# Kernel tuning notes

Measured on AMD Instinct MI355X. Metric: run time of the kernel, lower is better.

Reference implementation:

```python
import jax, jax.numpy as jnp
import numpy as np

DIM = 16  # scale_size[0] * scale_size[1]
SCALE = DIM ** -0.5


def setup_inputs() -> dict:
    key = jax.random.key(0)
    k1, k2 = jax.random.split(key)
    x = jax.random.normal(k1, (16, 256, 256, 64), dtype=jnp.float32)
    # torch Linear(dim, 2*dim, bias=False): weight shape [32, 16]
    w_qkv = jax.random.normal(k2, (32, 16), dtype=jnp.float32) * (DIM ** -0.5)
    return {"x": x, "w_qkv": w_qkv}


def reference(x, w_qkv):
    B, H, W, C = x.shape
    sh, sw = 4, 4  # scale_size
    # permute to (b, c, h, w) then adaptive avg pool to (4, 4)
    xp = jnp.transpose(x, (0, 3, 1, 2))  # [B, C, H, W]
    pooled = xp.reshape(B, C, sh, H // sh, sw, W // sw).mean(axis=(3, 5))  # [B, C, 4, 4]
    tokens = pooled.reshape(B, C, DIM)  # [B, C, 16]
    # to_qkv: Linear with weight [2*dim, dim] -> x @ W^T, then chunk
    qk = jnp.einsum('bcn,dn->bcd', tokens, w_qkv)  # [B, C, 32]
    q, k = qk[..., :DIM], qk[..., DIM:]  # each [B, C, 16]
    dots = jnp.einsum('bin,bjn->bij', q, k) * SCALE  # [B, C, C]
    attn = jax.nn.softmax(dots, axis=-1)  # [B, C, C]
    out = jnp.einsum('bhwc,btc->bhwt', x, attn)  # [B, H, W, C]
    return jax.nn.gelu(out, approximate=False)
```

## Files before the change

### kernel.cpp

```cpp
#include <hip/hip_runtime.h>
#include <math.h>
#include <cstddef>

#define BB   16
#define HH   256
#define WW   256
#define CC   64
#define NTOK 16
#define NDIM 16

#define PART_FLOATS (BB * NTOK * 16 * CC)
#define FRAG_USHORT_PER_B (8 * 64 * 8)

typedef short s16x8 __attribute__((ext_vector_type(8)));
typedef float f32x4 __attribute__((ext_vector_type(4)));

__device__ __forceinline__ unsigned short f2bf_rne(float f) {
    unsigned int u = __float_as_uint(f);
    return (unsigned short)((u + 0x7fffu + ((u >> 16) & 1u)) >> 16);
}

__global__ __launch_bounds__(256) void pool_partial(const float* __restrict__ x,
                                                    float* __restrict__ part) {
    const int blk = blockIdx.x;
    const int rc  = blk & 15;
    const int n   = (blk >> 4) & 15;
    const int b   = blk >> 8;
    const int ph  = n >> 2, pw = n & 3;
    const int t   = threadIdx.x;
    const int c4  = (t & 15) << 2;
    const int sub = t >> 4;

    const int h0 = ph * 64 + rc * 4;
    const int w0 = pw * 64;
    const float* xb = x + (((size_t)b * HH + h0) * WW + w0) * CC;

    float4 s = make_float4(0.f, 0.f, 0.f, 0.f);
#pragma unroll
    for (int k = 0; k < 16; ++k) {
        const int pos = sub + (k << 4);
        const int row = pos >> 6;
        const int col = pos & 63;
        const float4 v = *(const float4*)(xb + ((size_t)row * WW + col) * CC + c4);
        s.x += v.x; s.y += v.y; s.z += v.z; s.w += v.w;
    }

    __shared__ float lds[16 * 64];
    lds[sub * 64 + c4 + 0] = s.x;
    lds[sub * 64 + c4 + 1] = s.y;
    lds[sub * 64 + c4 + 2] = s.z;
    lds[sub * 64 + c4 + 3] = s.w;
    __syncthreads();

    if (t < 64) {
        float acc = 0.f;
#pragma unroll
        for (int ss = 0; ss < 16; ++ss) acc += lds[ss * 64 + t];
        part[(((size_t)b * NTOK + n) * 16 + rc) * CC + t] = acc;
    }
}

__global__ __launch_bounds__(256) void attn_kernel(const float* __restrict__ part,
                                                   const float* __restrict__ w_qkv,
                                                   unsigned short* __restrict__ fragw) {
    const int b = blockIdx.x;
    const int t = threadIdx.x;

    __shared__ float tok[CC * NDIM];
    __shared__ float ql [CC * NDIM];
    __shared__ float kl [CC * NDIM];
    __shared__ float dl [CC * CC];
    __shared__ float rs [CC];

    const float* pb = part + (size_t)b * NTOK * 16 * CC;

    {
        const int n  = t >> 4;
        const int cq = t & 15;
        float4 a = make_float4(0.f, 0.f, 0.f, 0.f);
#pragma unroll
        for (int rc = 0; rc < 16; ++rc) {
            const float4 v = *(const float4*)(pb + ((size_t)n * 16 + rc) * CC + cq * 4);
            a.x += v.x; a.y += v.y; a.z += v.z; a.w += v.w;
        }
        tok[(cq * 4 + 0) * NDIM + n] = a.x * (1.0f / 4096.0f);
        tok[(cq * 4 + 1) * NDIM + n] = a.y * (1.0f / 4096.0f);
        tok[(cq * 4 + 2) * NDIM + n] = a.z * (1.0f / 4096.0f);
        tok[(cq * 4 + 3) * NDIM + n] = a.w * (1.0f / 4096.0f);
    }
    __syncthreads();

    for (int idx = t; idx < CC * 32; idx += 256) {
        const int c = idx >> 5, d = idx & 31;
        float a = 0.f;
#pragma unroll
        for (int n = 0; n < NDIM; ++n) a += tok[c * NDIM + n] * w_qkv[d * NDIM + n];
        if (d < 16) ql[c * NDIM + d] = a;
        else        kl[c * NDIM + (d - 16)] = a;
    }
    __syncthreads();

    for (int idx = t; idx < CC * CC; idx += 256) {
        const int i = idx >> 6, j = idx & 63;
        float a = 0.f;
#pragma unroll
        for (int n = 0; n < NDIM; ++n) a += ql[i * NDIM + n] * kl[j * NDIM + n];
        dl[idx] = a * 0.25f;
    }
    __syncthreads();

    if (t < CC) {
        float m = -1e30f;
        for (int j = 0; j < CC; ++j) m = fmaxf(m, dl[t * CC + j]);
        float ssum = 0.f;
        for (int j = 0; j < CC; ++j) {
            const float e = expf(dl[t * CC + j] - m);
            dl[t * CC + j] = e;
            ssum += e;
        }
        rs[t] = 1.0f / ssum;
    }
    __syncthreads();

    for (int idx = t; idx < 512; idx += 256) {
        const int tt   = idx >> 3;
        const int oct  = idx & 7;
        const int ks   = oct >> 2;
        const int g    = oct & 3;
        const int slot = (tt >> 4) * 2 + ks;
        const int lanei = (tt & 15) + g * 16;
        const float rr = rs[tt];
        s16x8 hi;
#pragma unroll
        for (int j = 0; j < 8; ++j)
            hi[j] = (short)f2bf_rne(dl[tt * CC + oct * 8 + j] * rr);
        s16x8* dst = (s16x8*)fragw + ((size_t)b * 8 + slot) * 64;
        dst[lanei] = hi;
    }
}

__device__ __forceinline__ float gelu_fast(float v) {
    const float u = v * v;
    const float z = v * fmaf(0.07135482f, u, 1.59576912f);
    const float e = exp2f(z * -1.44269504f);
    return v * __builtin_amdgcn_rcpf(e + 1.0f);
}

__device__ __forceinline__ s16x8 pack8(const float4 a, const float4 b) {
    union { unsigned int u[4]; s16x8 v; } r;
    asm("v_cvt_pk_bf16_f32 %0, %1, %2" : "=v"(r.u[0]) : "v"(a.x), "v"(a.y));
    asm("v_cvt_pk_bf16_f32 %0, %1, %2" : "=v"(r.u[1]) : "v"(a.z), "v"(a.w));
    asm("v_cvt_pk_bf16_f32 %0, %1, %2" : "=v"(r.u[2]) : "v"(b.x), "v"(b.y));
    asm("v_cvt_pk_bf16_f32 %0, %1, %2" : "=v"(r.u[3]) : "v"(b.z), "v"(b.w));
    return r.v;
}

__global__ __launch_bounds__(256) void out_mfma(const float* __restrict__ x,
                                                const unsigned short* __restrict__ frag,
                                                float* __restrict__ out) {
    const int tid  = threadIdx.x;
    const int lane = tid & 63;
    const int wv   = tid >> 6;
    const int blk  = blockIdx.x;
    const int b    = blk >> 8;
    const int row  = lane & 15;
    const int g    = lane >> 4;

    const size_t pix0 = (size_t)blk * 256 + wv * 64;
    const float* xb = x + (pix0 + row) * CC + g * 8;

    float4 a0 = *(const float4*)(xb);
    float4 a1 = *(const float4*)(xb + 4);
    float4 a2 = *(const float4*)(xb + 32);
    float4 a3 = *(const float4*)(xb + 36);

    const s16x8* fb = (const s16x8*)(frag + (size_t)b * FRAG_USHORT_PER_B);
    s16x8 bf[8];
#pragma unroll
    for (int s = 0; s < 8; ++s) bf[s] = fb[s * 64 + lane];

    const float* x1 = xb + 16 * CC;
    float4 b0v = *(const float4*)(x1);
    float4 b1v = *(const float4*)(x1 + 4);
    float4 b2v = *(const float4*)(x1 + 32);
    float4 b3v = *(const float4*)(x1 + 36);

    float* ob = out + (pix0 + row) * CC + (g << 2);

#define TCOLS(PT, XH0, XH1)                                                      \
    _Pragma("unroll")                                                            \
    for (int tt = 0; tt < 4; ++tt) {                                             \
        f32x4 acc = {0.f, 0.f, 0.f, 0.f};                                        \
        acc = __builtin_amdgcn_mfma_f32_16x16x32_bf16(bf[tt * 2], XH0, acc, 0, 0, 0);     \
        acc = __builtin_amdgcn_mfma_f32_16x16x32_bf16(bf[tt * 2 + 1], XH1, acc, 0, 0, 0); \
        f32x4 gv;                                                                \
        gv.x = gelu_fast(acc.x); gv.y = gelu_fast(acc.y);                        \
        gv.z = gelu_fast(acc.z); gv.w = gelu_fast(acc.w);                        \
        *(f32x4*)(ob + (size_t)(PT) * 16 * CC + tt * 16) = gv;                   \
    }

    {
        const s16x8 xh0 = pack8(a0, a1);
        const s16x8 xh1 = pack8(a2, a3);
        const float* nx = xb + 32 * CC;
        a0 = *(const float4*)(nx);
        a1 = *(const float4*)(nx + 4);
        a2 = *(const float4*)(nx + 32);
        a3 = *(const float4*)(nx + 36);
        TCOLS(0, xh0, xh1)
    }
    {
        const s16x8 xh0 = pack8(b0v, b1v);
        const s16x8 xh1 = pack8(b2v, b3v);
        const float* nx = xb + 48 * CC;
        b0v = *(const float4*)(nx);
        b1v = *(const float4*)(nx + 4);
        b2v = *(const float4*)(nx + 32);
        b3v = *(const float4*)(nx + 36);
        TCOLS(1, xh0, xh1)
    }
    {
        const s16x8 xh0 = pack8(a0, a1);
        const s16x8 xh1 = pack8(a2, a3);
        TCOLS(2, xh0, xh1)
    }
    {
        const s16x8 xh0 = pack8(b0v, b1v);
        const s16x8 xh1 = pack8(b2v, b3v);
        TCOLS(3, xh0, xh1)
    }
#undef TCOLS
}

extern "C" void kernel_launch(void* const* d_in, const int* in_sizes, int n_in,
                              void* d_out, int out_size, void* d_ws, size_t ws_size,
                              hipStream_t stream) {
    const float* x     = (const float*)d_in[0];
    const float* w_qkv = (const float*)d_in[1];
    float* out   = (float*)d_out;
    float* part  = (float*)d_ws;
    unsigned short* frag = (unsigned short*)(part + PART_FLOATS);

    pool_partial<<<BB * NTOK * 16, 256, 0, stream>>>(x, part);
    attn_kernel<<<BB, 256, 0, stream>>>(part, w_qkv, frag);
    out_mfma<<<BB * 256, 256, 0, stream>>>(x, frag, out);
}
```

Baseline: 515.6 us.

## Split batch in halves and overlap output pass with next half's pooling

```diff
diff --git a/kernel.cpp b/kernel.cpp
--- a/kernel.cpp
+++ b/kernel.cpp
@@ -8,6 +8,7 @@
 #define CC   64
 #define NTOK 16
 #define NDIM 16
+#define HALF_B 8
 
 #define PART_FLOATS (BB * NTOK * 16 * CC)
 #define FRAG_USHORT_PER_B (8 * 64 * 8)
@@ -20,9 +21,8 @@
     return (unsigned short)((u + 0x7fffu + ((u >> 16) & 1u)) >> 16);
 }
 
-__global__ __launch_bounds__(256) void pool_partial(const float* __restrict__ x,
-                                                    float* __restrict__ part) {
-    const int blk = blockIdx.x;
+__device__ __forceinline__ void pool_body(const float* __restrict__ x,
+                                          float* __restrict__ part, int blk) {
     const int rc  = blk & 15;
     const int n   = (blk >> 4) & 15;
     const int b   = blk >> 8;
@@ -60,10 +60,17 @@
     }
 }
 
+__global__ __launch_bounds__(256) void pool_partial(const float* __restrict__ x,
+                                                    float* __restrict__ part,
+                                                    int b0) {
+    pool_body(x, part, b0 * 256 + (int)blockIdx.x);
+}
+
 __global__ __launch_bounds__(256) void attn_kernel(const float* __restrict__ part,
                                                    const float* __restrict__ w_qkv,
-                                                   unsigned short* __restrict__ fragw) {
-    const int b = blockIdx.x;
+                                                   unsigned short* __restrict__ fragw,
+                                                   int b0) {
+    const int b = b0 + blockIdx.x;
     const int t = threadIdx.x;
 
     __shared__ float tok[CC * NDIM];
@@ -155,13 +162,12 @@
     return r.v;
 }
 
-__global__ __launch_bounds__(256) void out_mfma(const float* __restrict__ x,
-                                                const unsigned short* __restrict__ frag,
-                                                float* __restrict__ out) {
+__device__ __forceinline__ void out_body(const float* __restrict__ x,
+                                         const unsigned short* __restrict__ frag,
+                                         float* __restrict__ out, int blk) {
     const int tid  = threadIdx.x;
     const int lane = tid & 63;
     const int wv   = tid >> 6;
-    const int blk  = blockIdx.x;
     const int b    = blk >> 8;
     const int row  = lane & 15;
     const int g    = lane >> 4;
@@ -180,10 +186,10 @@
     for (int s = 0; s < 8; ++s) bf[s] = fb[s * 64 + lane];
 
     const float* x1 = xb + 16 * CC;
-    float4 b0v = *(const float4*)(x1);
-    float4 b1v = *(const float4*)(x1 + 4);
-    float4 b2v = *(const float4*)(x1 + 32);
-    float4 b3v = *(const float4*)(x1 + 36);
+    float4 c0 = *(const float4*)(x1);
+    float4 c1 = *(const float4*)(x1 + 4);
+    float4 c2 = *(const float4*)(x1 + 32);
+    float4 c3 = *(const float4*)(x1 + 36);
 
     float* ob = out + (pix0 + row) * CC + (g << 2);
 
@@ -210,13 +216,13 @@
         TCOLS(0, xh0, xh1)
     }
     {
-        const s16x8 xh0 = pack8(b0v, b1v);
-        const s16x8 xh1 = pack8(b2v, b3v);
+        const s16x8 xh0 = pack8(c0, c1);
+        const s16x8 xh1 = pack8(c2, c3);
         const float* nx = xb + 48 * CC;
-        b0v = *(const float4*)(nx);
-        b1v = *(const float4*)(nx + 4);
-        b2v = *(const float4*)(nx + 32);
-        b3v = *(const float4*)(nx + 36);
+        c0 = *(const float4*)(nx);
+        c1 = *(const float4*)(nx + 4);
+        c2 = *(const float4*)(nx + 32);
+        c3 = *(const float4*)(nx + 36);
         TCOLS(1, xh0, xh1)
     }
     {
@@ -225,11 +231,28 @@
         TCOLS(2, xh0, xh1)
     }
     {
-        const s16x8 xh0 = pack8(b0v, b1v);
-        const s16x8 xh1 = pack8(b2v, b3v);
+        const s16x8 xh0 = pack8(c0, c1);
+        const s16x8 xh1 = pack8(c2, c3);
         TCOLS(3, xh0, xh1)
     }
 #undef TCOLS
+}
+
+__global__ __launch_bounds__(256) void out_mfma(const float* __restrict__ x,
+                                                const unsigned short* __restrict__ frag,
+                                                float* __restrict__ out,
+                                                int b0) {
+    out_body(x, frag, out, b0 * 256 + (int)blockIdx.x);
+}
+
+__global__ __launch_bounds__(256) void fused_out_pool(const float* __restrict__ x,
+                                                      const unsigned short* __restrict__ frag,
+                                                      float* __restrict__ out,
+                                                      float* __restrict__ part,
+                                                      int b0_out, int b0_pool) {
+    const int blk2 = (int)blockIdx.x;
+    if (blk2 & 1) pool_body(x, part, b0_pool * 256 + (blk2 >> 1));
+    else          out_body(x, frag, out, b0_out * 256 + (blk2 >> 1));
 }
 
 extern "C" void kernel_launch(void* const* d_in, const int* in_sizes, int n_in,
@@ -241,7 +264,9 @@
     float* part  = (float*)d_ws;
     unsigned short* frag = (unsigned short*)(part + PART_FLOATS);
 
-    pool_partial<<<BB * NTOK * 16, 256, 0, stream>>>(x, part);
-    attn_kernel<<<BB, 256, 0, stream>>>(part, w_qkv, frag);
-    out_mfma<<<BB * 256, 256, 0, stream>>>(x, frag, out);
-}
+    pool_partial<<<HALF_B * 256, 256, 0, stream>>>(x, part, 0);
+    attn_kernel<<<HALF_B, 256, 0, stream>>>(part, w_qkv, frag, 0);
+    fused_out_pool<<<2 * HALF_B * 256, 256, 0, stream>>>(x, frag, out, part, 0, HALF_B);
+    attn_kernel<<<HALF_B, 256, 0, stream>>>(part, w_qkv, frag, HALF_B);
+    out_mfma<<<HALF_B * 256, 256, 0, stream>>>(x, frag, out, HALF_B);
+}
```

Result: slower. 544.7 us (+5.6%).
